# Kernel optimization log

Measured on AMD Instinct MI355X. Metric: run time of the kernel, lower is better.

## Reference

```python
import jax, jax.numpy as jnp
import numpy as np

EPS = 1e-10

def setup_inputs() -> dict:
    key = jax.random.key(0)
    k1, k2 = jax.random.split(key)
    support_set = jax.random.normal(k1, (8192, 1024), dtype=jnp.float32)
    input_image = jax.random.normal(k2, (2048, 1024), dtype=jnp.float32)
    return {"support_set": support_set, "input_image": input_image}

def reference(support_set, input_image):
    # support_set: [n, d], input_image: [b, d]
    # Faithful to original: input magnitude is a single scalar over the whole
    # [b, d] input matrix; support magnitude is a scalar per support vector.
    input_mag = jax.lax.rsqrt(jnp.maximum(jnp.sum(input_image * input_image), EPS))  # scalar
    support_mag = jax.lax.rsqrt(jnp.maximum(jnp.sum(support_set * support_set, axis=1), EPS))  # [n]
    dot = jnp.einsum('bd,nd->nb', input_image, support_set)  # [n, b]
    sims = dot * support_mag[:, None] * input_mag  # [n, b]
    return sims[:, :, None]  # [n, b, 1] == torch.stack(...)[n,b,1].squeeze(1) (no-op for b>1)
```

## Files before the change

kernel.cpp:

```cpp
#include <hip/hip_runtime.h>
#include <hip/hip_bf16.h>
#include <stdint.h>
#include <stddef.h>

#define M_DIM 8192
#define N_DIM 2048
#define K_DIM 1024

#define BM 256
#define BN 256
#define BK 64
#define NKT (K_DIM / BK)
#define NITER (NKT / 2)

typedef __attribute__((ext_vector_type(8))) short short8;
typedef __attribute__((ext_vector_type(4))) float float4v;

static __device__ __forceinline__ unsigned short f2bf(float x) {
  union { float f; unsigned u; } c; c.f = x;
  return (unsigned short)((c.u + 0x7FFFu + ((c.u >> 16) & 1u)) >> 16);
}

#define GLOAD_LDS16(g, l)                                           \
  __builtin_amdgcn_global_load_lds(                                 \
      (const __attribute__((address_space(1))) void*)(g),           \
      (__attribute__((address_space(3))) void*)(l), 16, 0, 0)

__global__ __launch_bounds__(256) void prep(
    const float* __restrict__ S, const float* __restrict__ I,
    unsigned short* __restrict__ Sb, unsigned short* __restrict__ Ib,
    float* __restrict__ smag, float* __restrict__ partials) {
  const int t = threadIdx.x;
  const int lane = t & 63;
  const int wave = t >> 6;
  const int blk = blockIdx.x;
  const bool isS = blk < 2048;
  const int row = (isS ? blk : blk - 2048) * 4 + wave;
  const float* src = (isS ? S : I) + (size_t)row * K_DIM;
  unsigned short* dst = (isS ? Sb : Ib) + (size_t)row * K_DIM;

  float ss = 0.f;
#pragma unroll
  for (int i = 0; i < 4; ++i) {
    const float4 v = reinterpret_cast<const float4*>(src)[lane + i * 64];
    ushort4 b;
    b.x = f2bf(v.x); b.y = f2bf(v.y); b.z = f2bf(v.z); b.w = f2bf(v.w);
    reinterpret_cast<ushort4*>(dst)[lane + i * 64] = b;
    ss += v.x * v.x + v.y * v.y + v.z * v.z + v.w * v.w;
  }
#pragma unroll
  for (int m = 32; m >= 1; m >>= 1) ss += __shfl_xor(ss, m, 64);
  if (lane == 0) {
    if (isS) smag[row] = rsqrtf(fmaxf(ss, 1e-10f));
    else     partials[row] = ss;
  }
}

__global__ __launch_bounds__(512, 2) void gemm_bt(
    const unsigned short* __restrict__ A,
    const unsigned short* __restrict__ B,
    const float* __restrict__ smag,
    const float* __restrict__ partials,
    float* __restrict__ C) {
  __shared__ __align__(16) unsigned short lA[32768];
  __shared__ __align__(16) unsigned short lB[32768];
  __shared__ float wsum[8];

  const int t = threadIdx.x;
  const int lane = t & 63;
  const int wave = t >> 6;
  const int wr = wave >> 2;
  const int wc = wave & 3;

  const int blk = blockIdx.x;
  const int xcd = blk & 7;
  const int slot = blk >> 3;
  const int bm = (xcd * 4 + (slot & 3)) * BM;
  const int bn = (slot >> 2) * BN;

  {
    float p = partials[t] + partials[t + 512] + partials[t + 1024] + partials[t + 1536];
#pragma unroll
    for (int m = 32; m >= 1; m >>= 1) p += __shfl_xor(p, m, 64);
    if (lane == 0) wsum[wave] = p;
  }
  asm volatile("s_waitcnt vmcnt(0)" ::: "memory");

  const int srow = t >> 3;
  const int skc = (t & 7) ^ (srow & 7);
  const unsigned short* gA[4];
  const unsigned short* gB[4];
  int aoff[4];
#pragma unroll
  for (int j = 0; j < 4; ++j) {
    gA[j] = A + (size_t)(bm + j * 64 + srow) * K_DIM + skc * 8;
    gB[j] = B + (size_t)(bn + j * 64 + srow) * K_DIM + skc * 8;
    aoff[j] = (j >> 1) * 8192 + (j & 1) * 4096 + wave * 512;
  }

#define STAGE_A(j, buf) do { GLOAD_LDS16(gA[j], &lA[(buf) * 16384 + aoff[j]]); gA[j] += BK; } while (0)
#define STAGE_B(j, buf) do { GLOAD_LDS16(gB[j], &lB[(buf) * 16384 + aoff[j]]); gB[j] += BK; } while (0)
#define SP1(buf) do { STAGE_B(0, buf); STAGE_B(1, buf); } while (0)
#define SP2(buf) do { STAGE_B(2, buf); STAGE_B(3, buf); } while (0)
#define SP3(buf) do { STAGE_A(0, buf); STAGE_A(2, buf); } while (0)
#define SP4(buf) do { STAGE_A(1, buf); STAGE_A(3, buf); } while (0)

  const int fr = lane & 15;
  const int q = lane >> 4;
  const int pc0 = (q ^ (fr & 7)) * 8;
  const int pc1 = ((4 + q) ^ (fr & 7)) * 8;
  const unsigned short* rA = lA + wr * 8192 + fr * 64;
  const unsigned short* rB = lB + (wc >> 1) * 8192 + ((wc & 1) * 64 + fr) * 64;

  short8 afA[4], afB[4];
  short8 bf0[4], bf1[4];
  float4v acc[8][4];
#pragma unroll
  for (int i = 0; i < 8; ++i)
#pragma unroll
    for (int j = 0; j < 4; ++j) acc[i][j] = (float4v)0.0f;

#define BARRIER() __builtin_amdgcn_s_barrier()
#define VMW(n) asm volatile("s_waitcnt vmcnt(" #n ")" ::: "memory")
#define PRIO1() __builtin_amdgcn_s_setprio(1)
#define PRIO0() __builtin_amdgcn_s_setprio(0)

#define LA(bank, buf, half, s) do {                                            \
    _Pragma("unroll") for (int m = 0; m < 4; ++m)                              \
      bank[m] = *reinterpret_cast<const short8*>(                              \
          rA + (buf) * 16384 + ((half) * 4 + m) * 1024 + ((s) ? pc1 : pc0));   \
  } while (0)

#define LB2(bank, buf, s, j0) do {                                             \
    _Pragma("unroll") for (int n = 0; n < 2; ++n)                              \
      bank[(j0) + n] = *reinterpret_cast<const short8*>(                       \
          rB + (buf) * 16384 + ((j0) + n) * 1024 + ((s) ? pc1 : pc0));         \
  } while (0)

#define MQ(half, abank, bbank) do {                                            \
    PRIO1();                                                                   \
    _Pragma("unroll") for (int m = 0; m < 4; ++m)                              \
    _Pragma("unroll") for (int n = 0; n < 4; ++n)                              \
      acc[(half) * 4 + m][n] = __builtin_amdgcn_mfma_f32_16x16x32_bf16(        \
          abank[m], bbank[n], acc[(half) * 4 + m][n], 0, 0, 0);                \
    PRIO0();                                                                   \
  } while (0)

  SP1(0); SP2(0); SP3(0); SP4(0);
  SP1(1);
  VMW(2);
  BARRIER();
  LB2(bf0, 0, 0, 0); LB2(bf0, 0, 0, 2);
  LA(afA, 0, 0, 0);

#pragma unroll 1
  for (int it = 0; it < NITER - 1; ++it) {
     SP2(1); VMW(4); BARRIER(); LA(afB, 0, 1, 0); LB2(bf1, 0, 1, 0); MQ(0, afA, bf0);
     SP3(1); VMW(4); BARRIER(); LA(afA, 0, 0, 1); LB2(bf1, 0, 1, 2); MQ(1, afB, bf0);
     SP4(1); VMW(4); BARRIER(); LA(afB, 0, 1, 1); LB2(bf0, 1, 0, 0); MQ(0, afA, bf1);
     SP1(0); VMW(4); BARRIER(); LA(afA, 1, 0, 0); LB2(bf0, 1, 0, 2); MQ(1, afB, bf1);
     SP2(0); VMW(4); BARRIER(); LA(afB, 1, 1, 0); LB2(bf1, 1, 1, 0); MQ(0, afA, bf0);
     SP3(0); VMW(4); BARRIER(); LA(afA, 1, 0, 1); LB2(bf1, 1, 1, 2); MQ(1, afB, bf0);
     SP4(0); VMW(4); BARRIER(); LA(afB, 1, 1, 1); LB2(bf0, 0, 0, 0); MQ(0, afA, bf1);
     SP1(1); VMW(4); BARRIER(); LA(afA, 0, 0, 0); LB2(bf0, 0, 0, 2); MQ(1, afB, bf1);
  }
   SP2(1); VMW(4); BARRIER(); LA(afB, 0, 1, 0); LB2(bf1, 0, 1, 0); MQ(0, afA, bf0);
   SP3(1); VMW(4); BARRIER(); LA(afA, 0, 0, 1); LB2(bf1, 0, 1, 2); MQ(1, afB, bf0);
   SP4(1); VMW(4); BARRIER(); LA(afB, 0, 1, 1); LB2(bf0, 1, 0, 0); MQ(0, afA, bf1);
           VMW(2); BARRIER(); LA(afA, 1, 0, 0); LB2(bf0, 1, 0, 2); MQ(1, afB, bf1);
           VMW(0); BARRIER(); LA(afB, 1, 1, 0); LB2(bf1, 1, 1, 0); MQ(0, afA, bf0);
                   BARRIER(); LA(afA, 1, 0, 1); LB2(bf1, 1, 1, 2); MQ(1, afB, bf0);
                   BARRIER(); LA(afB, 1, 1, 1);                    MQ(0, afA, bf1);
                   BARRIER();                                      MQ(1, afB, bf1);

  const float imag = rsqrtf(fmaxf(wsum[0] + wsum[1] + wsum[2] + wsum[3] +
                                  wsum[4] + wsum[5] + wsum[6] + wsum[7], 1e-10f));
#pragma unroll
  for (int mi = 0; mi < 8; ++mi) {
    const int rbase = bm + wr * 128 + mi * 16 + q * 4;
#pragma unroll
    for (int r = 0; r < 4; ++r) {
      const int row = rbase + r;
      const float sc = smag[row] * imag;
      float* crow = C + (size_t)row * N_DIM + bn + wc * 64 + fr;
#pragma unroll
      for (int nj = 0; nj < 4; ++nj)
        __builtin_nontemporal_store(acc[mi][nj][r] * sc, crow + nj * 16);
    }
  }
}

extern "C" void kernel_launch(void* const* d_in, const int* in_sizes, int n_in,
                              void* d_out, int out_size, void* d_ws, size_t ws_size,
                              hipStream_t stream) {
  const float* S = (const float*)d_in[0];
  const float* I = (const float*)d_in[1];
  float* out = (float*)d_out;

  unsigned char* ws = (unsigned char*)d_ws;
  unsigned short* Sb = (unsigned short*)ws;
  unsigned short* Ib = (unsigned short*)(ws + (size_t)M_DIM * K_DIM * 2);
  float* smag = (float*)(ws + (size_t)M_DIM * K_DIM * 2 + (size_t)N_DIM * K_DIM * 2);
  float* partials = smag + M_DIM;

  hipLaunchKernelGGL(prep, dim3(2560), dim3(256), 0, stream,
                     S, I, Sb, Ib, smag, partials);
  hipLaunchKernelGGL(gemm_bt, dim3((M_DIM / BM) * (N_DIM / BN)), dim3(512), 0, stream,
                     Sb, Ib, smag, partials, out);
}
```

Measured before the change: 135.8 us.

## Deepen global prefetch by one stage and add sched_group_barrier MFMA/LDS interleave

Issues one more sub-stage of global-to-LDS loads ahead, relaxing vmcnt waits from 4 to 6 in the steady state, so memory latency has more time to be hidden. Adds sched_group_barrier hints that ask the compiler to group LDS reads and MFMA instructions in a fixed order within each phase. It also replaces nontemporal output stores with plain stores. The deeper prefetch depends on the buffer-reuse ordering still being safe, and the scheduling hints may constrain the compiler.

```diff
diff --git a/kernel.cpp b/kernel.cpp
--- a/kernel.cpp
+++ b/kernel.cpp
@@ -124,6 +124,14 @@
 #define VMW(n) asm volatile("s_waitcnt vmcnt(" #n ")" ::: "memory")
 #define PRIO1() __builtin_amdgcn_s_setprio(1)
 #define PRIO0() __builtin_amdgcn_s_setprio(0)
+#define SGB6() do {                                                            \
+    __builtin_amdgcn_sched_group_barrier(0x100, 6, 0);                         \
+    __builtin_amdgcn_sched_group_barrier(0x008, 16, 0);                        \
+  } while (0)
+#define SGB4() do {                                                            \
+    __builtin_amdgcn_sched_group_barrier(0x100, 4, 0);                         \
+    __builtin_amdgcn_sched_group_barrier(0x008, 16, 0);                        \
+  } while (0)
 
 #define LA(bank, buf, half, s) do {                                            \
     _Pragma("unroll") for (int m = 0; m < 4; ++m)                              \
@@ -147,31 +155,31 @@
   } while (0)
 
   SP1(0); SP2(0); SP3(0); SP4(0);
-  SP1(1);
-  VMW(2);
+  SP1(1); SP2(1);
+  VMW(6);
   BARRIER();
   LB2(bf0, 0, 0, 0); LB2(bf0, 0, 0, 2);
   LA(afA, 0, 0, 0);
 
 #pragma unroll 1
   for (int it = 0; it < NITER - 1; ++it) {
-     SP2(1); VMW(4); BARRIER(); LA(afB, 0, 1, 0); LB2(bf1, 0, 1, 0); MQ(0, afA, bf0);
-     SP3(1); VMW(4); BARRIER(); LA(afA, 0, 0, 1); LB2(bf1, 0, 1, 2); MQ(1, afB, bf0);
-     SP4(1); VMW(4); BARRIER(); LA(afB, 0, 1, 1); LB2(bf0, 1, 0, 0); MQ(0, afA, bf1);
-     SP1(0); VMW(4); BARRIER(); LA(afA, 1, 0, 0); LB2(bf0, 1, 0, 2); MQ(1, afB, bf1);
-     SP2(0); VMW(4); BARRIER(); LA(afB, 1, 1, 0); LB2(bf1, 1, 1, 0); MQ(0, afA, bf0);
-     SP3(0); VMW(4); BARRIER(); LA(afA, 1, 0, 1); LB2(bf1, 1, 1, 2); MQ(1, afB, bf0);
-     SP4(0); VMW(4); BARRIER(); LA(afB, 1, 1, 1); LB2(bf0, 0, 0, 0); MQ(0, afA, bf1);
-     SP1(1); VMW(4); BARRIER(); LA(afA, 0, 0, 0); LB2(bf0, 0, 0, 2); MQ(1, afB, bf1);
-  }
-   SP2(1); VMW(4); BARRIER(); LA(afB, 0, 1, 0); LB2(bf1, 0, 1, 0); MQ(0, afA, bf0);
-   SP3(1); VMW(4); BARRIER(); LA(afA, 0, 0, 1); LB2(bf1, 0, 1, 2); MQ(1, afB, bf0);
-   SP4(1); VMW(4); BARRIER(); LA(afB, 0, 1, 1); LB2(bf0, 1, 0, 0); MQ(0, afA, bf1);
-           VMW(2); BARRIER(); LA(afA, 1, 0, 0); LB2(bf0, 1, 0, 2); MQ(1, afB, bf1);
-           VMW(0); BARRIER(); LA(afB, 1, 1, 0); LB2(bf1, 1, 1, 0); MQ(0, afA, bf0);
-                   BARRIER(); LA(afA, 1, 0, 1); LB2(bf1, 1, 1, 2); MQ(1, afB, bf0);
-                   BARRIER(); LA(afB, 1, 1, 1);                    MQ(0, afA, bf1);
-                   BARRIER();                                      MQ(1, afB, bf1);
+     SP3(1); VMW(6); BARRIER(); SGB6(); LA(afB, 0, 1, 0); LB2(bf1, 0, 1, 0); MQ(0, afA, bf0);
+     SP4(1); VMW(6); BARRIER(); SGB6(); LA(afA, 0, 0, 1); LB2(bf1, 0, 1, 2); MQ(1, afB, bf0);
+     SP1(0); VMW(6); BARRIER(); SGB6(); LA(afB, 0, 1, 1); LB2(bf0, 1, 0, 0); MQ(0, afA, bf1);
+     SP2(0); VMW(6); BARRIER(); SGB6(); LA(afA, 1, 0, 0); LB2(bf0, 1, 0, 2); MQ(1, afB, bf1);
+     SP3(0); VMW(6); BARRIER(); SGB6(); LA(afB, 1, 1, 0); LB2(bf1, 1, 1, 0); MQ(0, afA, bf0);
+     SP4(0); VMW(6); BARRIER(); SGB6(); LA(afA, 1, 0, 1); LB2(bf1, 1, 1, 2); MQ(1, afB, bf0);
+     SP1(1); VMW(6); BARRIER(); SGB6(); LA(afB, 1, 1, 1); LB2(bf0, 0, 0, 0); MQ(0, afA, bf1);
+     SP2(1); VMW(6); BARRIER(); SGB6(); LA(afA, 0, 0, 0); LB2(bf0, 0, 0, 2); MQ(1, afB, bf1);
+  }
+   SP3(1); VMW(6); BARRIER(); SGB6(); LA(afB, 0, 1, 0); LB2(bf1, 0, 1, 0); MQ(0, afA, bf0);
+   SP4(1);         BARRIER(); SGB6(); LA(afA, 0, 0, 1); LB2(bf1, 0, 1, 2); MQ(1, afB, bf0);
+           VMW(4); BARRIER(); SGB6(); LA(afB, 0, 1, 1); LB2(bf0, 1, 0, 0); MQ(0, afA, bf1);
+           VMW(2); BARRIER(); SGB6(); LA(afA, 1, 0, 0); LB2(bf0, 1, 0, 2); MQ(1, afB, bf1);
+           VMW(0); BARRIER(); SGB6(); LA(afB, 1, 1, 0); LB2(bf1, 1, 1, 0); MQ(0, afA, bf0);
+                   BARRIER(); SGB6(); LA(afA, 1, 0, 1); LB2(bf1, 1, 1, 2); MQ(1, afB, bf0);
+                   BARRIER(); SGB4(); LA(afB, 1, 1, 1);                    MQ(0, afA, bf1);
+                   BARRIER();                                              MQ(1, afB, bf1);
 
   const float imag = rsqrtf(fmaxf(wsum[0] + wsum[1] + wsum[2] + wsum[3] +
                                   wsum[4] + wsum[5] + wsum[6] + wsum[7], 1e-10f));
@@ -184,8 +192,7 @@
       const float sc = smag[row] * imag;
       float* crow = C + (size_t)row * N_DIM + bn + wc * 64 + fr;
 #pragma unroll
-      for (int nj = 0; nj < 4; ++nj)
-        __builtin_nontemporal_store(acc[mi][nj][r] * sc, crow + nj * 16);
+      for (int nj = 0; nj < 4; ++nj) crow[nj * 16] = acc[mi][nj][r] * sc;
     }
   }
 }
```

Result: faster. 129.5 us (-4.7%).
